# Kernel optimization log

Hardware: AMD Instinct MI355X
Metric: run time of the kernel (lower is better)

## Reference

```python
import jax, jax.numpy as jnp
import numpy as np

EMBED_DIM = 128
ATTN_DIM = 64


def setup_inputs() -> dict:
    key = jax.random.key(0)
    kb, kt, kw1, kb1, kw2, kb2 = jax.random.split(key, 6)
    B, S, E = 2048, 200, EMBED_DIM
    behaviors = jax.random.normal(kb, (B, S, E), dtype=jnp.float32)
    target = jax.random.normal(kt, (B, E), dtype=jnp.float32)
    # Linear params (torch nn.Linear: y = x @ W.T + b); store as [in, out] for einsum
    lim1 = 1.0 / np.sqrt(4 * E)
    W1 = jax.random.uniform(kw1, (4 * E, ATTN_DIM), jnp.float32, -lim1, lim1)
    b1 = jax.random.uniform(kb1, (ATTN_DIM,), jnp.float32, -lim1, lim1)
    lim2 = 1.0 / np.sqrt(ATTN_DIM)
    W2 = jax.random.uniform(kw2, (ATTN_DIM, 1), jnp.float32, -lim2, lim2)
    b2 = jax.random.uniform(kb2, (1,), jnp.float32, -lim2, lim2)
    return {"behaviors": behaviors, "target": target, "W1": W1, "b1": b1, "W2": W2, "b2": b2}


def reference(behaviors, target, W1, b1, W2, b2):
    # behaviors: [B,S,E], target: [B,E] -> broadcast to [B,S,E]
    t = target[:, None, :]  # broadcast instead of repeat
    feat = jnp.concatenate([behaviors,
                            jnp.broadcast_to(t, behaviors.shape),
                            behaviors * t,
                            behaviors - t], axis=-1)  # [B,S,4E]
    h = jax.nn.relu(jnp.einsum('bsf,fa->bsa', feat, W1) + b1)  # [B,S,A]
    w = jax.nn.sigmoid(jnp.einsum('bsa,ao->bso', h, W2) + b2)  # [B,S,1]
    return jnp.sum(w * behaviors, axis=1)  # [B,E]
```

## Files before the change

### kernel.cpp

```cpp
#include <hip/hip_runtime.h>

typedef __attribute__((ext_vector_type(8))) short bf16x8;
typedef __attribute__((ext_vector_type(4))) float f32x4;

__device__ __forceinline__ short f2bf(float f) {
    union { float f; unsigned u; } v; v.f = f;
    unsigned r = (v.u + 0x7FFFu + ((v.u >> 16) & 1u)) >> 16;
    return (short)r;
}

__device__ __forceinline__ float sigmoidf(float x) {
    return 1.0f / (1.0f + __expf(-x));
}

constexpr int S = 200, E = 128, A = 64;
constexpr int NSTRIP = 13;

__global__ __launch_bounds__(256, 4) void attn_fused(
    const float* __restrict__ behaviors,
    const float* __restrict__ target,
    const float* __restrict__ W1,
    const float* __restrict__ b1,
    const float* __restrict__ W2,
    const float* __restrict__ b2,
    float* __restrict__ out)
{
    __shared__ short wb_f[16 * 512];
    __shared__ short wbtmp[E * A];
    __shared__ float red[4 * 128];
    __shared__ float t_lds[E];
    __shared__ float bias_lds[A];
    __shared__ float w2_lds[A];

    const int tid  = threadIdx.x;
    const int bat  = blockIdx.x;
    const int lane = tid & 63;
    const int wave = tid >> 6;
    const int l15  = lane & 15;
    const int quad = lane >> 4;

    if (tid < E) t_lds[tid] = target[(size_t)bat * E + tid];
    __syncthreads();

    for (int i = tid; i < E * A; i += 256) {
        const int e = i >> 6, a = i & 63;
        wbtmp[i] = f2bf(W1[e * A + a] + W1[(384 + e) * A + a]
                        + t_lds[e] * W1[(256 + e) * A + a]);
    }
    {
        const int a = tid & 63, seg = tid >> 6;
        float acc = 0.f;
        for (int e = seg * 32; e < seg * 32 + 32; ++e)
            acc += t_lds[e] * (W1[(128 + e) * A + a] - W1[(384 + e) * A + a]);
        red[seg * 64 + a] = acc;
    }
    __syncthreads();
    if (tid < A) {
        bias_lds[tid] = b1[tid] + red[tid] + red[64 + tid] + red[128 + tid] + red[192 + tid];
        w2_lds[tid] = W2[tid];
    }
    for (int i = tid; i < E * A; i += 256) {
        const int j = i & 7, ln = (i >> 3) & 63, frag = i >> 9;
        const int kt = frag >> 2, nt = frag & 3;
        const int n = nt * 16 + (ln & 15);
        const int k = kt * 32 + (ln >> 4) * 8 + j;
        wb_f[i] = wbtmp[k * A + n];
    }
    __syncthreads();

    float bias_l[4], w2_l[4];
    #pragma unroll
    for (int nt = 0; nt < 4; ++nt) {
        bias_l[nt] = bias_lds[nt * 16 + l15];
        w2_l[nt]   = w2_lds[nt * 16 + l15];
    }
    const float b2v = b2[0];
    const float* bptr = behaviors + (size_t)bat * S * E;

    f32x4 oacc[4][2];
    #pragma unroll
    for (int kt = 0; kt < 4; ++kt) {
        oacc[kt][0] = f32x4{0.f, 0.f, 0.f, 0.f};
        oacc[kt][1] = f32x4{0.f, 0.f, 0.f, 0.f};
    }

    for (int st = wave; st < NSTRIP; st += 4) {
        const int row = st * 16 + l15;
        const bool valid = (row < S);
        const float* rp = bptr + (size_t)row * E + quad * 8;

        f32x4 av[4][2];
        #pragma unroll
        for (int kt = 0; kt < 4; ++kt) {
            av[kt][0] = f32x4{0.f, 0.f, 0.f, 0.f};
            av[kt][1] = f32x4{0.f, 0.f, 0.f, 0.f};
        }
        if (valid) {
            #pragma unroll
            for (int kt = 0; kt < 4; ++kt) {
                av[kt][0] = *(const f32x4*)(rp + kt * 32);
                av[kt][1] = *(const f32x4*)(rp + kt * 32 + 4);
            }
        }

        f32x4 acc[4];
        #pragma unroll
        for (int nt = 0; nt < 4; ++nt) acc[nt] = f32x4{0.f, 0.f, 0.f, 0.f};

        #pragma unroll
        for (int kt = 0; kt < 4; ++kt) {
            bf16x8 af;
            af[0] = f2bf(av[kt][0][0]); af[1] = f2bf(av[kt][0][1]);
            af[2] = f2bf(av[kt][0][2]); af[3] = f2bf(av[kt][0][3]);
            af[4] = f2bf(av[kt][1][0]); af[5] = f2bf(av[kt][1][1]);
            af[6] = f2bf(av[kt][1][2]); af[7] = f2bf(av[kt][1][3]);
            #pragma unroll
            for (int nt = 0; nt < 4; ++nt) {
                bf16x8 bf = *(const bf16x8*)&wb_f[(kt * 4 + nt) * 512 + lane * 8];
                acc[nt] = __builtin_amdgcn_mfma_f32_16x16x32_bf16(af, bf, acc[nt], 0, 0, 0);
            }
        }

        float wgt[4];
        #pragma unroll
        for (int reg = 0; reg < 4; ++reg) {
            float p = 0.f;
            #pragma unroll
            for (int nt = 0; nt < 4; ++nt) {
                const float h = acc[nt][reg] + bias_l[nt];
                p += fmaxf(h, 0.f) * w2_l[nt];
            }
            p += __shfl_xor(p, 1, 64);
            p += __shfl_xor(p, 2, 64);
            p += __shfl_xor(p, 4, 64);
            p += __shfl_xor(p, 8, 64);
            wgt[reg] = sigmoidf(p + b2v);
        }

        const int srcl = (l15 >> 2) << 4;
        const float t0 = __shfl(wgt[0], srcl, 64);
        const float t1 = __shfl(wgt[1], srcl, 64);
        const float t2 = __shfl(wgt[2], srcl, 64);
        const float t3 = __shfl(wgt[3], srcl, 64);
        const float wl = (l15 & 2) ? ((l15 & 1) ? t3 : t2)
                                   : ((l15 & 1) ? t1 : t0);

        #pragma unroll
        for (int kt = 0; kt < 4; ++kt) {
            #pragma unroll
            for (int h = 0; h < 2; ++h) {
                oacc[kt][h][0] += wl * av[kt][h][0];
                oacc[kt][h][1] += wl * av[kt][h][1];
                oacc[kt][h][2] += wl * av[kt][h][2];
                oacc[kt][h][3] += wl * av[kt][h][3];
            }
        }
    }

    #pragma unroll
    for (int kt = 0; kt < 4; ++kt)
        #pragma unroll
        for (int h = 0; h < 2; ++h)
            #pragma unroll
            for (int c = 0; c < 4; ++c) {
                float v = oacc[kt][h][c];
                v += __shfl_xor(v, 1, 64);
                v += __shfl_xor(v, 2, 64);
                v += __shfl_xor(v, 4, 64);
                v += __shfl_xor(v, 8, 64);
                oacc[kt][h][c] = v;
            }

    if (l15 == 0) {
        #pragma unroll
        for (int kt = 0; kt < 4; ++kt) {
            *(f32x4*)&red[wave * 128 + kt * 32 + quad * 8]     = oacc[kt][0];
            *(f32x4*)&red[wave * 128 + kt * 32 + quad * 8 + 4] = oacc[kt][1];
        }
    }
    __syncthreads();
    if (tid < E) {
        out[(size_t)bat * E + tid] =
            red[tid] + red[128 + tid] + red[256 + tid] + red[384 + tid];
    }
}

extern "C" void kernel_launch(void* const* d_in, const int* in_sizes, int n_in,
                              void* d_out, int out_size, void* d_ws, size_t ws_size,
                              hipStream_t stream) {
    const float* behaviors = (const float*)d_in[0];
    const float* target    = (const float*)d_in[1];
    const float* W1        = (const float*)d_in[2];
    const float* b1        = (const float*)d_in[3];
    const float* W2        = (const float*)d_in[4];
    const float* b2        = (const float*)d_in[5];
    float* out = (float*)d_out;

    hipLaunchKernelGGL(attn_fused, dim3(2048), dim3(256), 0, stream,
                       behaviors, target, W1, b1, W2, b2, out);
}
```

Measured before the change: 355.1 us.

## Hoist per-batch weight folding into a precompute kernel and double the MFMA K

Adds a separate precompute kernel that builds a batch-independent bf16 weight fragment layout (two K halves: behaviors and behaviors*target) and a per-batch bias vector. The main kernel no longer recomputes a target-dependent folded weight matrix per block; it copies the pre-laid-out fragments into LDS and multiplies behaviors*target on the fly, doubling MFMA work. Behavior loads use nontemporal hints, and occupancy drops to 3 waves per SIMD because LDS use grows. This trades the heavy per-block prologue (W1 reads, transposes, syncs) for extra MFMAs and a second kernel launch.

Measured after the change: 465.9 us. 31.2% more time.

```diff
diff --git a/kernel.cpp b/kernel.cpp
--- a/kernel.cpp
+++ b/kernel.cpp
@@ -2,6 +2,7 @@
 
 typedef __attribute__((ext_vector_type(8))) short bf16x8;
 typedef __attribute__((ext_vector_type(4))) float f32x4;
+typedef __attribute__((ext_vector_type(4))) unsigned int u32x4;
 
 __device__ __forceinline__ short f2bf(float f) {
     union { float f; unsigned u; } v; v.f = f;
@@ -15,22 +16,50 @@
 
 constexpr int S = 200, E = 128, A = 64;
 constexpr int NSTRIP = 13;
-
-__global__ __launch_bounds__(256, 4) void attn_fused(
-    const float* __restrict__ behaviors,
+constexpr int WFRAG_SHORTS = 16384;
+
+__global__ __launch_bounds__(256) void precomp(
     const float* __restrict__ target,
     const float* __restrict__ W1,
     const float* __restrict__ b1,
+    short* __restrict__ wfrag,
+    float* __restrict__ beta)
+{
+    const int tid = threadIdx.x;
+    if (blockIdx.x == 512) {
+        for (int i = tid; i < WFRAG_SHORTS; i += 256) {
+            const int j = i & 7, ln = (i >> 3) & 63, f = i >> 9;
+            const int kt = f >> 2, nt = f & 3;
+            const int n = nt * 16 + (ln & 15);
+            const int k = kt * 32 + (ln >> 4) * 8 + j;
+            const float v = (k < 128)
+                ? W1[k * A + n] + W1[(384 + k) * A + n]
+                : W1[(128 + k) * A + n];
+            wfrag[i] = f2bf(v);
+        }
+    } else {
+        const int b = blockIdx.x * 4 + (tid >> 6);
+        const int a = tid & 63;
+        const float* tp = target + (size_t)b * E;
+        float acc = b1[a];
+        #pragma unroll 8
+        for (int e = 0; e < E; ++e)
+            acc += tp[e] * (W1[(128 + e) * A + a] - W1[(384 + e) * A + a]);
+        beta[b * A + a] = acc;
+    }
+}
+
+__global__ __launch_bounds__(256, 3) void attn_fused(
+    const float* __restrict__ behaviors,
+    const float* __restrict__ target,
     const float* __restrict__ W2,
     const float* __restrict__ b2,
+    const short* __restrict__ wfrag,
+    const float* __restrict__ beta,
     float* __restrict__ out)
 {
-    __shared__ short wb_f[16 * 512];
-    __shared__ short wbtmp[E * A];
+    __shared__ short wb_f[WFRAG_SHORTS];
     __shared__ float red[4 * 128];
-    __shared__ float t_lds[E];
-    __shared__ float bias_lds[A];
-    __shared__ float w2_lds[A];
 
     const int tid  = threadIdx.x;
     const int bat  = blockIdx.x;
@@ -39,43 +68,31 @@
     const int l15  = lane & 15;
     const int quad = lane >> 4;
 
-    if (tid < E) t_lds[tid] = target[(size_t)bat * E + tid];
-    __syncthreads();
-
-    for (int i = tid; i < E * A; i += 256) {
-        const int e = i >> 6, a = i & 63;
-        wbtmp[i] = f2bf(W1[e * A + a] + W1[(384 + e) * A + a]
-                        + t_lds[e] * W1[(256 + e) * A + a]);
-    }
     {
-        const int a = tid & 63, seg = tid >> 6;
-        float acc = 0.f;
-        for (int e = seg * 32; e < seg * 32 + 32; ++e)
-            acc += t_lds[e] * (W1[(128 + e) * A + a] - W1[(384 + e) * A + a]);
-        red[seg * 64 + a] = acc;
-    }
-    __syncthreads();
-    if (tid < A) {
-        bias_lds[tid] = b1[tid] + red[tid] + red[64 + tid] + red[128 + tid] + red[192 + tid];
-        w2_lds[tid] = W2[tid];
-    }
-    for (int i = tid; i < E * A; i += 256) {
-        const int j = i & 7, ln = (i >> 3) & 63, frag = i >> 9;
-        const int kt = frag >> 2, nt = frag & 3;
-        const int n = nt * 16 + (ln & 15);
-        const int k = kt * 32 + (ln >> 4) * 8 + j;
-        wb_f[i] = wbtmp[k * A + n];
-    }
-    __syncthreads();
+        const u32x4* src = (const u32x4*)wfrag;
+        u32x4* dst = (u32x4*)wb_f;
+        #pragma unroll
+        for (int i = 0; i < 8; ++i) dst[tid + i * 256] = src[tid + i * 256];
+    }
+
+    const float* tp = target + (size_t)bat * E;
+    f32x4 tv[4][2];
+    #pragma unroll
+    for (int kt = 0; kt < 4; ++kt) {
+        tv[kt][0] = *(const f32x4*)(tp + kt * 32 + quad * 8);
+        tv[kt][1] = *(const f32x4*)(tp + kt * 32 + quad * 8 + 4);
+    }
 
     float bias_l[4], w2_l[4];
     #pragma unroll
     for (int nt = 0; nt < 4; ++nt) {
-        bias_l[nt] = bias_lds[nt * 16 + l15];
-        w2_l[nt]   = w2_lds[nt * 16 + l15];
+        bias_l[nt] = beta[(size_t)bat * A + nt * 16 + l15];
+        w2_l[nt]   = W2[nt * 16 + l15];
     }
     const float b2v = b2[0];
     const float* bptr = behaviors + (size_t)bat * S * E;
+
+    __syncthreads();
 
     f32x4 oacc[4][2];
     #pragma unroll
@@ -98,8 +115,8 @@
         if (valid) {
             #pragma unroll
             for (int kt = 0; kt < 4; ++kt) {
-                av[kt][0] = *(const f32x4*)(rp + kt * 32);
-                av[kt][1] = *(const f32x4*)(rp + kt * 32 + 4);
+                av[kt][0] = __builtin_nontemporal_load((const f32x4*)(rp + kt * 32));
+                av[kt][1] = __builtin_nontemporal_load((const f32x4*)(rp + kt * 32 + 4));
             }
         }
 
@@ -109,15 +126,24 @@
 
         #pragma unroll
         for (int kt = 0; kt < 4; ++kt) {
-            bf16x8 af;
-            af[0] = f2bf(av[kt][0][0]); af[1] = f2bf(av[kt][0][1]);
-            af[2] = f2bf(av[kt][0][2]); af[3] = f2bf(av[kt][0][3]);
-            af[4] = f2bf(av[kt][1][0]); af[5] = f2bf(av[kt][1][1]);
-            af[6] = f2bf(av[kt][1][2]); af[7] = f2bf(av[kt][1][3]);
+            bf16x8 af, af2;
+            #pragma unroll
+            for (int h = 0; h < 2; ++h) {
+                #pragma unroll
+                for (int c = 0; c < 4; ++c) {
+                    af[h * 4 + c]  = f2bf(av[kt][h][c]);
+                    af2[h * 4 + c] = f2bf(av[kt][h][c] * tv[kt][h][c]);
+                }
+            }
             #pragma unroll
             for (int nt = 0; nt < 4; ++nt) {
-                bf16x8 bf = *(const bf16x8*)&wb_f[(kt * 4 + nt) * 512 + lane * 8];
-                acc[nt] = __builtin_amdgcn_mfma_f32_16x16x32_bf16(af, bf, acc[nt], 0, 0, 0);
+                bf16x8 bf1 = *(const bf16x8*)&wb_f[(kt * 4 + nt) * 512 + lane * 8];
+                acc[nt] = __builtin_amdgcn_mfma_f32_16x16x32_bf16(af, bf1, acc[nt], 0, 0, 0);
+            }
+            #pragma unroll
+            for (int nt = 0; nt < 4; ++nt) {
+                bf16x8 bf2 = *(const bf16x8*)&wb_f[((kt + 4) * 4 + nt) * 512 + lane * 8];
+                acc[nt] = __builtin_amdgcn_mfma_f32_16x16x32_bf16(af2, bf2, acc[nt], 0, 0, 0);
             }
         }
 
@@ -196,6 +222,11 @@
     const float* b2        = (const float*)d_in[5];
     float* out = (float*)d_out;
 
+    short* wfrag = (short*)d_ws;
+    float* beta  = (float*)((char*)d_ws + WFRAG_SHORTS * sizeof(short));
+
+    hipLaunchKernelGGL(precomp, dim3(513), dim3(256), 0, stream,
+                       target, W1, b1, wfrag, beta);
     hipLaunchKernelGGL(attn_fused, dim3(2048), dim3(256), 0, stream,
-                       behaviors, target, W1, b1, W2, b2, out);
-}
+                       behaviors, target, W2, b2, wfrag, beta, out);
+}
```

## Prefetch behavior strips with double-buffered registers and overlap with weight prep

Applied to the files above, without the earlier changes.

Issues the first strip load of behaviors before the per-block weight folding and LDS setup, so global memory latency overlaps that prologue. The strip loop is fully unrolled with two register buffers, so each iteration prefetches the next strip while running MFMA on the current one. This raises register pressure (two 32-float buffers per thread) under launch_bounds(256,4), which may cause spills or lower occupancy.

After: 354.0 us. No clear change (-0.3%).

```diff
diff --git a/kernel.cpp b/kernel.cpp
--- a/kernel.cpp
+++ b/kernel.cpp
@@ -15,6 +15,25 @@
 
 constexpr int S = 200, E = 128, A = 64;
 constexpr int NSTRIP = 13;
+
+__device__ __forceinline__ void load_strip(f32x4 av[4][2], const float* __restrict__ bptr,
+                                           int st, int l15, int quad)
+{
+    #pragma unroll
+    for (int kt = 0; kt < 4; ++kt) {
+        av[kt][0] = f32x4{0.f, 0.f, 0.f, 0.f};
+        av[kt][1] = f32x4{0.f, 0.f, 0.f, 0.f};
+    }
+    const int row = st * 16 + l15;
+    if (st < NSTRIP && row < S) {
+        const float* rp = bptr + (size_t)row * E + quad * 8;
+        #pragma unroll
+        for (int kt = 0; kt < 4; ++kt) {
+            av[kt][0] = *(const f32x4*)(rp + kt * 32);
+            av[kt][1] = *(const f32x4*)(rp + kt * 32 + 4);
+        }
+    }
+}
 
 __global__ __launch_bounds__(256, 4) void attn_fused(
     const float* __restrict__ behaviors,
@@ -39,6 +58,11 @@
     const int l15  = lane & 15;
     const int quad = lane >> 4;
 
+    const float* bptr = behaviors + (size_t)bat * S * E;
+
+    f32x4 avA[4][2], avB[4][2];
+    load_strip(avA, bptr, wave, l15, quad);
+
     if (tid < E) t_lds[tid] = target[(size_t)bat * E + tid];
     __syncthreads();
 
@@ -50,6 +74,7 @@
     {
         const int a = tid & 63, seg = tid >> 6;
         float acc = 0.f;
+        #pragma unroll 8
         for (int e = seg * 32; e < seg * 32 + 32; ++e)
             acc += t_lds[e] * (W1[(128 + e) * A + a] - W1[(384 + e) * A + a]);
         red[seg * 64 + a] = acc;
@@ -60,8 +85,8 @@
         w2_lds[tid] = W2[tid];
     }
     for (int i = tid; i < E * A; i += 256) {
-        const int j = i & 7, ln = (i >> 3) & 63, frag = i >> 9;
-        const int kt = frag >> 2, nt = frag & 3;
+        const int j = i & 7, ln = (i >> 3) & 63, f = i >> 9;
+        const int kt = f >> 2, nt = f & 3;
         const int n = nt * 16 + (ln & 15);
         const int k = kt * 32 + (ln >> 4) * 8 + j;
         wb_f[i] = wbtmp[k * A + n];
@@ -75,7 +100,6 @@
         w2_l[nt]   = w2_lds[nt * 16 + l15];
     }
     const float b2v = b2[0];
-    const float* bptr = behaviors + (size_t)bat * S * E;
 
     f32x4 oacc[4][2];
     #pragma unroll
@@ -84,24 +108,13 @@
         oacc[kt][1] = f32x4{0.f, 0.f, 0.f, 0.f};
     }
 
-    for (int st = wave; st < NSTRIP; st += 4) {
-        const int row = st * 16 + l15;
-        const bool valid = (row < S);
-        const float* rp = bptr + (size_t)row * E + quad * 8;
-
-        f32x4 av[4][2];
-        #pragma unroll
-        for (int kt = 0; kt < 4; ++kt) {
-            av[kt][0] = f32x4{0.f, 0.f, 0.f, 0.f};
-            av[kt][1] = f32x4{0.f, 0.f, 0.f, 0.f};
-        }
-        if (valid) {
-            #pragma unroll
-            for (int kt = 0; kt < 4; ++kt) {
-                av[kt][0] = *(const f32x4*)(rp + kt * 32);
-                av[kt][1] = *(const f32x4*)(rp + kt * 32 + 4);
-            }
-        }
+    #pragma unroll
+    for (int it = 0; it < 4; ++it) {
+        const int st = wave + it * 4;
+        if (st >= NSTRIP) break;
+        f32x4 (*cur)[2] = (it & 1) ? avB : avA;
+        f32x4 (*nxt)[2] = (it & 1) ? avA : avB;
+        load_strip(nxt, bptr, st + 4, l15, quad);
 
         f32x4 acc[4];
         #pragma unroll
@@ -110,14 +123,15 @@
         #pragma unroll
         for (int kt = 0; kt < 4; ++kt) {
             bf16x8 af;
-            af[0] = f2bf(av[kt][0][0]); af[1] = f2bf(av[kt][0][1]);
-            af[2] = f2bf(av[kt][0][2]); af[3] = f2bf(av[kt][0][3]);
-            af[4] = f2bf(av[kt][1][0]); af[5] = f2bf(av[kt][1][1]);
-            af[6] = f2bf(av[kt][1][2]); af[7] = f2bf(av[kt][1][3]);
+            #pragma unroll
+            for (int h = 0; h < 2; ++h)
+                #pragma unroll
+                for (int c = 0; c < 4; ++c)
+                    af[h * 4 + c] = f2bf(cur[kt][h][c]);
             #pragma unroll
             for (int nt = 0; nt < 4; ++nt) {
-                bf16x8 bf = *(const bf16x8*)&wb_f[(kt * 4 + nt) * 512 + lane * 8];
-                acc[nt] = __builtin_amdgcn_mfma_f32_16x16x32_bf16(af, bf, acc[nt], 0, 0, 0);
+                bf16x8 bf1 = *(const bf16x8*)&wb_f[(kt * 4 + nt) * 512 + lane * 8];
+                acc[nt] = __builtin_amdgcn_mfma_f32_16x16x32_bf16(af, bf1, acc[nt], 0, 0, 0);
             }
         }
 
@@ -146,15 +160,14 @@
                                    : ((l15 & 1) ? t1 : t0);
 
         #pragma unroll
-        for (int kt = 0; kt < 4; ++kt) {
+        for (int kt = 0; kt < 4; ++kt)
             #pragma unroll
             for (int h = 0; h < 2; ++h) {
-                oacc[kt][h][0] += wl * av[kt][h][0];
-                oacc[kt][h][1] += wl * av[kt][h][1];
-                oacc[kt][h][2] += wl * av[kt][h][2];
-                oacc[kt][h][3] += wl * av[kt][h][3];
-            }
-        }
+                oacc[kt][h][0] += wl * cur[kt][h][0];
+                oacc[kt][h][1] += wl * cur[kt][h][1];
+                oacc[kt][h][2] += wl * cur[kt][h][2];
+                oacc[kt][h][3] += wl * cur[kt][h][3];
+            }
     }
 
     #pragma unroll
```
